# Kernel optimization log

Measured on AMD Instinct MI355X. Metric: run time of the kernel, lower is better.

Reference implementation:

```python
import jax, jax.numpy as jnp
import numpy as np

BN_EPS = 1e-5


def _poly_ste(x):
    # Piecewise polynomial surrogate used for the activation STE backward:
    #   x < -1        -> -1
    #   x >= 1        -> 1
    out = jnp.where(x < -1, -1.0, x * x + 2.0 * x)
    out = jnp.where(x < 0, out, -x * x + 2.0 * x)
    out = jnp.where(x < 1, out, 1.0)
    return out


def setup_inputs() -> dict:
    key = jax.random.key(0)
    ks = jax.random.split(key, 7)
    N, C, H, W = 32, 128, 56, 56
    P = 128  # planes
    return {
        "x": jax.random.normal(ks[0], (N, C, H, W), dtype=jnp.float32),
        "weight": jax.random.normal(ks[1], (P, C, 3, 3), dtype=jnp.float32) * 0.05,
        "bias": jax.random.normal(ks[2], (P,), dtype=jnp.float32) * 0.05,
        "gamma": jax.random.uniform(ks[3], (P,), dtype=jnp.float32, minval=0.5, maxval=1.5),
        "beta": jax.random.normal(ks[4], (P,), dtype=jnp.float32) * 0.05,
        "running_mean": jax.random.normal(ks[5], (P,), dtype=jnp.float32) * 0.1,
        "running_var": jax.random.uniform(ks[6], (P,), dtype=jnp.float32, minval=0.5, maxval=1.5),
    }


def reference(x, weight, bias, gamma, beta, running_mean, running_var):
    # BinaryActivation: forward = sign(x), backward = d(poly)/dx (STE via detach trick)
    poly = _poly_ste(x)
    a = poly + jax.lax.stop_gradient(jnp.sign(x) - poly)

    # HardBinaryConv: weights binarized with straight-through sign; input already +/-1.
    wb = weight + jax.lax.stop_gradient(jnp.sign(weight) - weight)

    # 3x3 conv, stride 1, padding 1, NCHW / OIHW layout
    out = jax.lax.conv_general_dilated(
        a, wb,
        window_strides=(1, 1),
        padding=((1, 1), (1, 1)),
        dimension_numbers=("NCHW", "OIHW", "NCHW"),
    )
    out = out + bias[None, :, None, None]

    # BatchNorm2d in eval mode (running statistics)
    inv = gamma / jnp.sqrt(running_var + BN_EPS)
    out = out * inv[None, :, None, None] + (beta - running_mean * inv)[None, :, None, None]

    # Residual add (downsample=None, stride=1, inplanes==planes)
    return out + x
```

## Files before the change

kernel.cpp:

```cpp
#include <hip/hip_runtime.h>
#include <stdint.h>

#define N_  32
#define C_  128
#define H_  56
#define W_  56
#define HW_ 3136
#define P_  128
#define NPIX (N_*HW_)

using i32x4 = __attribute__((ext_vector_type(4))) int;

#define ABITS_BYTES (NPIX*16)
#define WI8_BYTES   (P_*1152)

__global__ __launch_bounds__(256) void pack_x_kernel(const float* __restrict__ x,
                                                     uint32_t* __restrict__ abits_w) {
    int b      = blockIdx.x;
    int j      = b & 3;
    int pairId = (b >> 2) * 256 + threadIdx.x;
    int n      = pairId / (HW_ / 2);
    int r      = (pairId % (HW_ / 2)) * 2;
    const float* px = x + ((size_t)n * C_ + j * 32) * HW_ + r;
    uint32_t w0 = 0, w1 = 0;
    #pragma unroll
    for (int c = 0; c < 32; ++c) {
        float2 v = *(const float2*)(px + (size_t)c * HW_);
        if (v.x >= 0.f) w0 |= 1u << c;
        if (v.y >= 0.f) w1 |= 1u << c;
    }
    int pix = n * HW_ + r;
    abits_w[(size_t)pix * 4 + j]       = w0;
    abits_w[(size_t)(pix + 1) * 4 + j] = w1;
}

__global__ __launch_bounds__(256) void wpack_kernel(const float* __restrict__ weight,
        const float* __restrict__ bias, const float* __restrict__ gamma,
        const float* __restrict__ beta, const float* __restrict__ mean,
        const float* __restrict__ var,
        uint32_t* __restrict__ wI8, float* __restrict__ invG, float* __restrict__ b0G) {
    int gid = blockIdx.x * 256 + threadIdx.x;
    int p   = gid / 288;
    int rem = gid % 288;
    int k   = rem * 4;
    int tp  = k >> 7;
    int c   = k & 127;
    uint32_t d = 0;
    #pragma unroll
    for (int i2 = 0; i2 < 4; ++i2) {
        float v = weight[((size_t)p * C_ + c + i2) * 9 + tp];
        uint32_t by = (v >= 0.f) ? 0x01u : 0xFFu;
        d |= by << (8 * i2);
    }
    wI8[gid] = d;
    if (blockIdx.x == 0 && threadIdx.x < P_) {
        int pp = threadIdx.x;
        float inv = gamma[pp] * rsqrtf(var[pp] + 1e-5f);
        invG[pp] = inv;
        b0G[pp]  = bias[pp] * inv + beta[pp] - mean[pp] * inv;
    }
}

__global__ __launch_bounds__(256) void bconv_kernel(
        const uint4* __restrict__ abits, const uint4* __restrict__ wI8v,
        const float* __restrict__ invG, const float* __restrict__ b0G,
        const float* __restrict__ x, float* __restrict__ out) {
    __shared__ uint4 actT[4 * 68 * 8];
    __shared__ float sInv[P_], sB0[P_];

    int tid = threadIdx.x;
    int img = blockIdx.x / 28;
    int rp  = blockIdx.x % 28;
    int r0  = rp * 2;

    if (tid < P_) { sInv[tid] = invG[tid]; sB0[tid] = b0G[tid]; }

    for (int cell = tid; cell < 4 * 68; cell += 256) {
        int rho  = cell & 3;
        int colL = cell >> 2;
        int h    = r0 - 1 + rho;
        int wv   = colL - 1;
        bool valid = ((unsigned)h < H_) && ((unsigned)wv < W_);
        uint4 bits = valid ? abits[img * HW_ + h * W_ + wv] : make_uint4(0u, 0u, 0u, 0u);
        uint32_t bwv[4] = {bits.x, bits.y, bits.z, bits.w};
        int base16 = (rho * 68 + colL) * 8;
        int sz = colL & 7;
        #pragma unroll
        for (int cb = 0; cb < 8; ++cb) {
            uint32_t hw16 = (bwv[cb >> 1] >> ((cb & 1) * 16)) & 0xFFFFu;
            uint4 dq;
            uint32_t n0 = hw16 & 0xF, n1 = (hw16 >> 4) & 0xF,
                     n2 = (hw16 >> 8) & 0xF, n3 = (hw16 >> 12) & 0xF;
            dq.x = 0xFFFFFFFFu ^ (((n0 * 0x204081u) & 0x01010101u) * 0xFEu);
            dq.y = 0xFFFFFFFFu ^ (((n1 * 0x204081u) & 0x01010101u) * 0xFEu);
            dq.z = 0xFFFFFFFFu ^ (((n2 * 0x204081u) & 0x01010101u) * 0xFEu);
            dq.w = 0xFFFFFFFFu ^ (((n3 * 0x204081u) & 0x01010101u) * 0xFEu);
            if (!valid) { dq.x = dq.y = dq.z = dq.w = 0u; }
            actT[base16 + (cb ^ sz)] = dq;
        }
    }

    int lane = tid & 63;
    int wi   = tid >> 6;
    int q    = lane >> 4;
    int l15  = lane & 15;
    int m0   = wi * 32;

    i32x4 aw[2][2][2];
    #pragma unroll
    for (int mi = 0; mi < 2; ++mi)
        #pragma unroll
        for (int ks = 0; ks < 2; ++ks)
            aw[0][mi][ks] = *(const i32x4*)&wI8v[(size_t)(m0 + mi*16 + l15) * 72
                                                 + 0 * 8 + ks * 4 + q];

    i32x4 acc[2][8];
    #pragma unroll
    for (int mi = 0; mi < 2; ++mi)
        #pragma unroll
        for (int j = 0; j < 8; ++j)
            #pragma unroll
            for (int e = 0; e < 4; ++e) acc[mi][j][e] = 0;

    __syncthreads();

    for (int t9 = 0; t9 < 9; ++t9) {
        int nb = t9 & 1;
        if (t9 < 8) {
            #pragma unroll
            for (int mi = 0; mi < 2; ++mi)
                #pragma unroll
                for (int ks = 0; ks < 2; ++ks)
                    aw[nb ^ 1][mi][ks] = *(const i32x4*)&wI8v[(size_t)(m0 + mi*16 + l15) * 72
                                                              + (t9 + 1) * 8 + ks * 4 + q];
        }
        int dh = t9 / 3, dw = t9 % 3;
        #pragma unroll
        for (int ks = 0; ks < 2; ++ks) {
            #pragma unroll
            for (int j = 0; j < 8; ++j) {
                int n    = j * 16 + l15;
                int colL = (n & 63) + dw;
                int rho  = (n >> 6) + dh;
                i32x4 bf = *(const i32x4*)&actT[(rho * 68 + colL) * 8 + ((ks * 4 + q) ^ (colL & 7))];
                acc[0][j] = __builtin_amdgcn_mfma_i32_16x16x64_i8(aw[nb][0][ks], bf, acc[0][j], 0, 0, 0);
                acc[1][j] = __builtin_amdgcn_mfma_i32_16x16x64_i8(aw[nb][1][ks], bf, acc[1][j], 0, 0, 0);
            }
        }
    }

    float invR[2][4], b0R[2][4];
    #pragma unroll
    for (int mi = 0; mi < 2; ++mi)
        #pragma unroll
        for (int reg = 0; reg < 4; ++reg) {
            int m = m0 + mi * 16 + q * 4 + reg;
            invR[mi][reg] = sInv[m];
            b0R[mi][reg]  = sB0[m];
        }
    #pragma unroll
    for (int j = 0; j < 8; ++j) {
        int n = j * 16 + l15;
        int w = n & 63;
        if (w < W_) {
            int orow = r0 + (n >> 6);
            size_t pixOff = (size_t)img * P_ * HW_ + (size_t)orow * W_ + w;
            #pragma unroll
            for (int mi = 0; mi < 2; ++mi)
                #pragma unroll
                for (int reg = 0; reg < 4; ++reg) {
                    int m = m0 + mi * 16 + q * 4 + reg;
                    size_t off = pixOff + (size_t)m * HW_;
                    out[off] = (float)acc[mi][j][reg] * invR[mi][reg] + b0R[mi][reg] + x[off];
                }
        }
    }
}

extern "C" void kernel_launch(void* const* d_in, const int* in_sizes, int n_in,
                              void* d_out, int out_size, void* d_ws, size_t ws_size,
                              hipStream_t stream) {
    const float* x      = (const float*)d_in[0];
    const float* weight = (const float*)d_in[1];
    const float* bias   = (const float*)d_in[2];
    const float* gamma  = (const float*)d_in[3];
    const float* beta   = (const float*)d_in[4];
    const float* mean   = (const float*)d_in[5];
    const float* var    = (const float*)d_in[6];
    float* out = (float*)d_out;

    uint8_t*  ws    = (uint8_t*)d_ws;
    uint32_t* abits = (uint32_t*)ws;
    uint32_t* wI8   = (uint32_t*)(ws + ABITS_BYTES);
    float*    invG  = (float*)(ws + ABITS_BYTES + WI8_BYTES);
    float*    b0G   = invG + P_;

    pack_x_kernel<<<(NPIX / 2) * 4 / 256, 256, 0, stream>>>(x, abits);
    wpack_kernel<<<144, 256, 0, stream>>>(weight, bias, gamma, beta, mean, var, wI8, invG, b0G);
    bconv_kernel<<<32 * 28, 256, 0, stream>>>((const uint4*)abits, (const uint4*)wI8,
                                              invG, b0G, x, out);
}
```

Before: 150.4 us.

## Fuse activation binarization into conv kernel, reading x directly per tile

```diff
diff --git a/kernel.cpp b/kernel.cpp
--- a/kernel.cpp
+++ b/kernel.cpp
@@ -7,32 +7,10 @@
 #define W_  56
 #define HW_ 3136
 #define P_  128
-#define NPIX (N_*HW_)
 
 using i32x4 = __attribute__((ext_vector_type(4))) int;
 
-#define ABITS_BYTES (NPIX*16)
-#define WI8_BYTES   (P_*1152)
-
-__global__ __launch_bounds__(256) void pack_x_kernel(const float* __restrict__ x,
-                                                     uint32_t* __restrict__ abits_w) {
-    int b      = blockIdx.x;
-    int j      = b & 3;
-    int pairId = (b >> 2) * 256 + threadIdx.x;
-    int n      = pairId / (HW_ / 2);
-    int r      = (pairId % (HW_ / 2)) * 2;
-    const float* px = x + ((size_t)n * C_ + j * 32) * HW_ + r;
-    uint32_t w0 = 0, w1 = 0;
-    #pragma unroll
-    for (int c = 0; c < 32; ++c) {
-        float2 v = *(const float2*)(px + (size_t)c * HW_);
-        if (v.x >= 0.f) w0 |= 1u << c;
-        if (v.y >= 0.f) w1 |= 1u << c;
-    }
-    int pix = n * HW_ + r;
-    abits_w[(size_t)pix * 4 + j]       = w0;
-    abits_w[(size_t)(pix + 1) * 4 + j] = w1;
-}
+#define WI8_BYTES (P_*1152)
 
 __global__ __launch_bounds__(256) void wpack_kernel(const float* __restrict__ weight,
         const float* __restrict__ bias, const float* __restrict__ gamma,
@@ -61,8 +39,8 @@
     }
 }
 
-__global__ __launch_bounds__(256) void bconv_kernel(
-        const uint4* __restrict__ abits, const uint4* __restrict__ wI8v,
+__global__ __launch_bounds__(256, 4) void bconv_kernel(
+        const uint4* __restrict__ wI8v,
         const float* __restrict__ invG, const float* __restrict__ b0G,
         const float* __restrict__ x, float* __restrict__ out) {
     __shared__ uint4 actT[4 * 68 * 8];
@@ -72,33 +50,6 @@
     int img = blockIdx.x / 28;
     int rp  = blockIdx.x % 28;
     int r0  = rp * 2;
-
-    if (tid < P_) { sInv[tid] = invG[tid]; sB0[tid] = b0G[tid]; }
-
-    for (int cell = tid; cell < 4 * 68; cell += 256) {
-        int rho  = cell & 3;
-        int colL = cell >> 2;
-        int h    = r0 - 1 + rho;
-        int wv   = colL - 1;
-        bool valid = ((unsigned)h < H_) && ((unsigned)wv < W_);
-        uint4 bits = valid ? abits[img * HW_ + h * W_ + wv] : make_uint4(0u, 0u, 0u, 0u);
-        uint32_t bwv[4] = {bits.x, bits.y, bits.z, bits.w};
-        int base16 = (rho * 68 + colL) * 8;
-        int sz = colL & 7;
-        #pragma unroll
-        for (int cb = 0; cb < 8; ++cb) {
-            uint32_t hw16 = (bwv[cb >> 1] >> ((cb & 1) * 16)) & 0xFFFFu;
-            uint4 dq;
-            uint32_t n0 = hw16 & 0xF, n1 = (hw16 >> 4) & 0xF,
-                     n2 = (hw16 >> 8) & 0xF, n3 = (hw16 >> 12) & 0xF;
-            dq.x = 0xFFFFFFFFu ^ (((n0 * 0x204081u) & 0x01010101u) * 0xFEu);
-            dq.y = 0xFFFFFFFFu ^ (((n1 * 0x204081u) & 0x01010101u) * 0xFEu);
-            dq.z = 0xFFFFFFFFu ^ (((n2 * 0x204081u) & 0x01010101u) * 0xFEu);
-            dq.w = 0xFFFFFFFFu ^ (((n3 * 0x204081u) & 0x01010101u) * 0xFEu);
-            if (!valid) { dq.x = dq.y = dq.z = dq.w = 0u; }
-            actT[base16 + (cb ^ sz)] = dq;
-        }
-    }
 
     int lane = tid & 63;
     int wi   = tid >> 6;
@@ -106,6 +57,8 @@
     int l15  = lane & 15;
     int m0   = wi * 32;
 
+    if (tid < P_) { sInv[tid] = invG[tid]; sB0[tid] = b0G[tid]; }
+
     i32x4 aw[2][2][2];
     #pragma unroll
     for (int mi = 0; mi < 2; ++mi)
@@ -113,6 +66,64 @@
         for (int ks = 0; ks < 2; ++ks)
             aw[0][mi][ks] = *(const i32x4*)&wI8v[(size_t)(m0 + mi*16 + l15) * 72
                                                  + 0 * 8 + ks * 4 + q];
+
+    if (tid < 224) {
+        int rho = tid / 56;
+        int rr  = tid % 56;
+        int cg  = rr / 14;
+        int tq  = rr % 14;
+        int h   = r0 - 1 + rho;
+        bool vh = ((unsigned)h < (unsigned)H_);
+        uint32_t dwv[4][8];
+        #pragma unroll
+        for (int k2 = 0; k2 < 4; ++k2)
+            #pragma unroll
+            for (int d = 0; d < 8; ++d) dwv[k2][d] = 0;
+        if (vh) {
+            const uint32_t* xb = (const uint32_t*)x
+                + ((size_t)img * C_ + cg * 32) * HW_ + h * W_ + tq * 4;
+            #pragma unroll
+            for (int ci = 0; ci < 32; ++ci) {
+                uint4 u = *(const uint4*)(xb + (size_t)ci * HW_);
+                int d  = ci >> 2;
+                int sh = (ci & 3) * 8;
+                dwv[0][d] |= (u.x >> 31) << sh;
+                dwv[1][d] |= (u.y >> 31) << sh;
+                dwv[2][d] |= (u.z >> 31) << sh;
+                dwv[3][d] |= (u.w >> 31) << sh;
+            }
+        }
+        uint32_t c0 = vh ? 0x01010101u : 0u;
+        uint32_t cf = vh ? 0xFEu       : 0u;
+        int colL0 = tq * 4 + 1;
+        #pragma unroll
+        for (int k2 = 0; k2 < 4; ++k2) {
+            int colL = colL0 + k2;
+            int base = (rho * 68 + colL) * 8;
+            int sz   = colL & 7;
+            uint4 lo, hi;
+            lo.x = c0 + dwv[k2][0] * cf;  lo.y = c0 + dwv[k2][1] * cf;
+            lo.z = c0 + dwv[k2][2] * cf;  lo.w = c0 + dwv[k2][3] * cf;
+            hi.x = c0 + dwv[k2][4] * cf;  hi.y = c0 + dwv[k2][5] * cf;
+            hi.z = c0 + dwv[k2][6] * cf;  hi.w = c0 + dwv[k2][7] * cf;
+            actT[base + ((2 * cg)     ^ sz)] = lo;
+            actT[base + ((2 * cg + 1) ^ sz)] = hi;
+        }
+    } else {
+        int z = tid - 224;
+        #pragma unroll
+        for (int rep = 0; rep < 2; ++rep) {
+            int e = z + rep * 32;
+            if (e < 48) {
+                int rho  = e / 12;
+                int jj   = e % 12;
+                int colL = jj ? (56 + jj) : 0;
+                int base = (rho * 68 + colL) * 8;
+                #pragma unroll
+                for (int s = 0; s < 8; ++s) actT[base + s] = make_uint4(0u,0u,0u,0u);
+            }
+        }
+    }
 
     i32x4 acc[2][8];
     #pragma unroll
@@ -190,13 +201,10 @@
     float* out = (float*)d_out;
 
     uint8_t*  ws    = (uint8_t*)d_ws;
-    uint32_t* abits = (uint32_t*)ws;
-    uint32_t* wI8   = (uint32_t*)(ws + ABITS_BYTES);
-    float*    invG  = (float*)(ws + ABITS_BYTES + WI8_BYTES);
+    uint32_t* wI8   = (uint32_t*)ws;
+    float*    invG  = (float*)(ws + WI8_BYTES);
     float*    b0G   = invG + P_;
 
-    pack_x_kernel<<<(NPIX / 2) * 4 / 256, 256, 0, stream>>>(x, abits);
     wpack_kernel<<<144, 256, 0, stream>>>(weight, bias, gamma, beta, mean, var, wI8, invG, b0G);
-    bconv_kernel<<<32 * 28, 256, 0, stream>>>((const uint4*)abits, (const uint4*)wI8,
-                                              invG, b0G, x, out);
+    bconv_kernel<<<32 * 28, 256, 0, stream>>>((const uint4*)wI8, invG, b0G, x, out);
 }
```

Result: slower. 205.7 us (+36.7%).
